# Optimization experiments

Hardware: AMD Instinct MI355X
Metric: run time of the kernel (lower is better)

## Reference

```python
import jax, jax.numpy as jnp
import numpy as np

N, E, D = 50000, 600000, 128


def setup_inputs() -> dict:
    key = jax.random.key(0)
    ks = jax.random.split(key, 7)
    s = 1.0 / np.sqrt(D)
    return {
        "x": jax.random.normal(ks[0], (N, D), dtype=jnp.float32),
        "edge_index": jax.random.randint(ks[1], (2, E), 0, N, dtype=jnp.int64),
        "Wl1": jax.random.normal(ks[2], (D, D), dtype=jnp.float32) * s,
        "Wr1": jax.random.normal(ks[3], (D, D), dtype=jnp.float32) * s,
        "b1": jnp.zeros((D,), dtype=jnp.float32),
        "Wl2": jax.random.normal(ks[4], (D, D), dtype=jnp.float32) * s,
        "Wr2": jax.random.normal(ks[5], (D, D), dtype=jnp.float32) * s,
        "b2": jnp.zeros((D,), dtype=jnp.float32),
    }


def _sage_conv(h, edge_index, Wl, Wr, b):
    # PyG SAGEConv (mean aggr): out = lin_l(mean_{j in N(i)} h_j) + lin_r(h_i)
    src, dst = edge_index[0], edge_index[1]
    n = h.shape[0]
    msg = h[src]                                            # [E, D] gather
    agg = jax.ops.segment_sum(msg, dst, num_segments=n)     # [N, D] scatter-add
    cnt = jax.ops.segment_sum(jnp.ones((src.shape[0],), h.dtype), dst,
                              num_segments=n)               # in-degree
    agg = agg / jnp.maximum(cnt, 1.0)[:, None]              # mean (0 for isolated)
    return agg @ Wl + h @ Wr + b


def reference(x, edge_index, Wl1, Wr1, b1, Wl2, Wr2, b2):
    h = jax.nn.relu(_sage_conv(x, edge_index, Wl1, Wr1, b1))
    # F.dropout(p=0.5) is identity in eval mode (deterministic baseline)
    return _sage_conv(h, edge_index, Wl2, Wr2, b2)
```

## Files before the change

### kernel.cpp

```cpp
#include <hip/hip_runtime.h>

typedef unsigned int u32;
typedef unsigned short u16;
typedef __attribute__((ext_vector_type(8))) short bf16x8;
typedef __attribute__((ext_vector_type(4))) float f32x4;

__device__ __forceinline__ u32 f2bf(float f) {
  u32 x = __float_as_uint(f);
  return (x + 0x7fffu + ((x >> 16) & 1u)) >> 16;
}
__device__ __forceinline__ float bf2f(u16 u) {
  return __uint_as_float(((u32)u) << 16);
}
__device__ __forceinline__ void addbf8(float* a, uint4 v) {
  a[0] += bf2f((u16)v.x); a[1] += bf2f((u16)(v.x >> 16));
  a[2] += bf2f((u16)v.y); a[3] += bf2f((u16)(v.y >> 16));
  a[4] += bf2f((u16)v.z); a[5] += bf2f((u16)(v.z >> 16));
  a[6] += bf2f((u16)v.w); a[7] += bf2f((u16)(v.w >> 16));
}

__global__ void setup_kernel(const float* __restrict__ Wl1, const float* __restrict__ Wr1,
                             const float* __restrict__ Wl2, const float* __restrict__ Wr2,
                             u16* __restrict__ G1, u16* __restrict__ G2,
                             int* __restrict__ cnt, int n) {
  int b = blockIdx.x;
  if (b < 256) {
    const float* Wl = (b < 128) ? Wl1 : Wl2;
    const float* Wr = (b < 128) ? Wr1 : Wr2;
    u16* G = (b < 128) ? G1 : G2;
    int id = (b & 127) * 256 + threadIdx.x;
    int c = id >> 7;
    int k = id & 127;
    const float* W = (c < 128) ? Wl : Wr;
    float v = W[k * 128 + (c & 127)];
    G[c * 128 + (k ^ ((c & 7) << 3))] = (u16)f2bf(v);
  } else {
    int i = (b - 256) * 256 + threadIdx.x;
    if (i < n) cnt[i] = 0;
  }
}

__global__ void hist_kernel(const int* __restrict__ dst, int* __restrict__ cnt,
                            int* __restrict__ pos, int E) {
  int e = blockIdx.x * blockDim.x + threadIdx.x;
  if (e < E) pos[e] = atomicAdd(&cnt[dst[e]], 1);
}

#define SCAN_CHUNK 2048

__global__ __launch_bounds__(256) void scan_sums(const int* __restrict__ cnt,
                                                 int* __restrict__ bsum, int n) {
  __shared__ int red[256];
  int t = threadIdx.x;
  int base = blockIdx.x * SCAN_CHUNK + t * 8;
  int s = 0;
#pragma unroll
  for (int i = 0; i < 8; ++i) {
    int idx = base + i;
    if (idx < n) s += cnt[idx];
  }
  red[t] = s;
  __syncthreads();
  for (int off = 128; off > 0; off >>= 1) {
    if (t < off) red[t] += red[t + off];
    __syncthreads();
  }
  if (t == 0) bsum[blockIdx.x] = red[0];
}

__global__ __launch_bounds__(256) void scan_apply(
    const int* __restrict__ cnt, const int* __restrict__ bsum, int nb,
    int* __restrict__ row_ptr, float* __restrict__ inv_cnt, int n) {
  __shared__ int sc[256];
  __shared__ int base_s;
  int t = threadIdx.x;
  if (t == 0) {
    int run = 0;
    int bid = blockIdx.x;
    int base = 0;
    for (int i = 0; i < nb; ++i) {
      if (i == bid) base = run;
      run += bsum[i];
    }
    base_s = base;
    if (bid == 0) row_ptr[n] = run;
  }
  int chunk_base = blockIdx.x * SCAN_CHUNK + t * 8;
  int v[8];
  int s = 0;
#pragma unroll
  for (int i = 0; i < 8; ++i) {
    int idx = chunk_base + i;
    v[i] = (idx < n) ? cnt[idx] : 0;
    s += v[i];
  }
  sc[t] = s;
  __syncthreads();
  for (int off = 1; off < 256; off <<= 1) {
    int add = (t >= off) ? sc[t - off] : 0;
    __syncthreads();
    sc[t] += add;
    __syncthreads();
  }
  int run = base_s + ((t > 0) ? sc[t - 1] : 0);
#pragma unroll
  for (int i = 0; i < 8; ++i) {
    int idx = chunk_base + i;
    if (idx < n) {
      row_ptr[idx] = run;
      inv_cnt[idx] = 1.0f / (float)max(v[i], 1);
      run += v[i];
    }
  }
}

template <int IN_BF16>
__device__ __forceinline__ void gemm_tiles(const void* in_, const u16* __restrict__ G,
                                           const float* __restrict__ bias,
                                           u16* __restrict__ yl, u16* __restrict__ yr,
                                           int n, uint4* lds4, int gb) {
  char* As = (char*)lds4;
  char* Bt = (char*)lds4 + 16384;
  const int t = threadIdx.x;
  const int lane = t & 63;
  const int wave = t >> 6;
  const int wr = wave >> 1;
  const int wc = wave & 1;
  const int lhi = lane >> 4;
  const int llo = lane & 15;

  {
    const uint4* gbp = (const uint4*)G;
    uint4* lb = lds4 + 1024;
#pragma unroll
    for (int i = 0; i < 16; ++i) lb[i * 256 + t] = gbp[i * 256 + t];
  }

  const int ntiles = (n + 63) / 64;
#pragma unroll 1
  for (int tile = gb * 2; tile < ntiles && tile < gb * 2 + 2; ++tile) {
    const int row0 = tile * 64;
    __syncthreads();
#pragma unroll
    for (int i = 0; i < 4; ++i) {
      int g = t + i * 256;
      int r = g >> 4;
      int gc = g & 15;
      int row = row0 + r;
      uint4 pk = {0u, 0u, 0u, 0u};
      if (row < n) {
        if (IN_BF16) {
          pk = *(const uint4*)((const u16*)in_ + (size_t)row * 128 + gc * 8);
        } else {
          const float4* pp = (const float4*)((const float*)in_ + (size_t)row * 128 + gc * 8);
          float4 v0 = pp[0], v1 = pp[1];
          pk.x = f2bf(v0.x) | (f2bf(v0.y) << 16);
          pk.y = f2bf(v0.z) | (f2bf(v0.w) << 16);
          pk.z = f2bf(v1.x) | (f2bf(v1.y) << 16);
          pk.w = f2bf(v1.z) | (f2bf(v1.w) << 16);
        }
      }
      *(uint4*)(As + r * 256 + ((gc * 16) ^ ((r & 7) << 4))) = pk;
    }
    __syncthreads();

    f32x4 acc[2][8];
#pragma unroll
    for (int fr = 0; fr < 2; ++fr)
#pragma unroll
      for (int fc = 0; fc < 8; ++fc) acc[fr][fc] = {0.f, 0.f, 0.f, 0.f};

#pragma unroll
    for (int ks = 0; ks < 4; ++ks) {
      const int kbyte = ks * 64 + lhi * 16;
      bf16x8 a[2], bb[8];
#pragma unroll
      for (int fr = 0; fr < 2; ++fr) {
        int r = wr * 32 + fr * 16 + llo;
        a[fr] = *(const bf16x8*)(As + r * 256 + (kbyte ^ ((r & 7) << 4)));
      }
#pragma unroll
      for (int fc = 0; fc < 8; ++fc) {
        int c = wc * 128 + fc * 16 + llo;
        bb[fc] = *(const bf16x8*)(Bt + c * 256 + (kbyte ^ ((c & 7) << 4)));
      }
#pragma unroll
      for (int fr = 0; fr < 2; ++fr)
#pragma unroll
        for (int fc = 0; fc < 8; ++fc)
          acc[fr][fc] = __builtin_amdgcn_mfma_f32_16x16x32_bf16(a[fr], bb[fc], acc[fr][fc], 0, 0, 0);
    }

#pragma unroll 1
    for (int ph = 0; ph < 2; ++ph) {
      __syncthreads();
      if (wc == ph) {
#pragma unroll
        for (int fc = 0; fc < 8; ++fc) {
          int cc = fc * 16 + llo;
          float bv = (ph == 1) ? bias[cc] : 0.0f;
#pragma unroll
          for (int fr = 0; fr < 2; ++fr) {
#pragma unroll
            for (int i = 0; i < 4; ++i) {
              int row = wr * 32 + fr * 16 + lhi * 4 + i;
              *(u16*)(As + row * 256 + ((cc * 2) ^ (lhi << 5))) =
                  (u16)f2bf(acc[fr][fc][i] + bv);
            }
          }
        }
      }
      __syncthreads();
      u16* outp = (ph == 0) ? yl : yr;
#pragma unroll
      for (int j = 0; j < 4; ++j) {
        int idx = t + j * 256;
        int row = idx >> 4;
        int cb = (idx & 15) * 16;
        int grow = row0 + row;
        if (grow < n) {
          uint4 v = *(const uint4*)(As + row * 256 + (cb ^ (((row >> 2) & 3) << 5)));
          *(uint4*)((char*)(outp + (size_t)grow * 128) + cb) = v;
        }
      }
    }
  }
}

__global__ __launch_bounds__(256, 2) void gemm1_fill_kernel(
    const float* __restrict__ x, const u16* __restrict__ G1, const float* __restrict__ b1,
    u16* __restrict__ yl, u16* __restrict__ yr, int n,
    const int* __restrict__ src, const int* __restrict__ dst,
    const int* __restrict__ pos, const int* __restrict__ row_ptr,
    int* __restrict__ colv, int E, int GB) {
  __shared__ uint4 lds4[5120];
  if ((int)blockIdx.x < GB) {
    gemm_tiles<0>(x, G1, b1, yl, yr, n, lds4, blockIdx.x);
  } else {
    int base = ((int)blockIdx.x - GB) * 2048 + threadIdx.x;
    int dd[8], pp[8], ss[8], rp[8];
#pragma unroll
    for (int j = 0; j < 8; ++j) {
      int e = base + j * 256;
      if (e < E) { dd[j] = dst[e]; pp[j] = pos[e]; ss[j] = src[e]; }
    }
#pragma unroll
    for (int j = 0; j < 8; ++j) {
      int e = base + j * 256;
      if (e < E) rp[j] = row_ptr[dd[j]];
    }
#pragma unroll
    for (int j = 0; j < 8; ++j) {
      int e = base + j * 256;
      if (e < E) colv[rp[j] + pp[j]] = ss[j];
    }
  }
}

template <int IN_BF16>
__global__ __launch_bounds__(256, 2) void gemm_kernel(
    const void* __restrict__ in_, const u16* __restrict__ G, const float* __restrict__ bias,
    u16* __restrict__ yl, u16* __restrict__ yr, int n) {
  __shared__ uint4 lds4[5120];
  gemm_tiles<IN_BF16>(in_, G, bias, yl, yr, n, lds4, blockIdx.x);
}

template <int RELU, int OUT_BF16>
__global__ __launch_bounds__(256) void agg_kernel(
    const u16* __restrict__ yl, const u16* __restrict__ yr,
    const int* __restrict__ row_ptr, const int* __restrict__ colv,
    const float* __restrict__ invc, void* __restrict__ out_, int n) {
  int node = blockIdx.x * 16 + (threadIdx.x >> 4);
  if (node >= n) return;
  int sl = threadIdx.x & 15;
  int beg = row_ptr[node], end = row_ptr[node + 1];
  uint4 rv = *(const uint4*)(yr + (size_t)node * 128 + sl * 8);
  float s = invc[node];
  float a[8] = {0.f, 0.f, 0.f, 0.f, 0.f, 0.f, 0.f, 0.f};
  for (int e0 = beg; e0 < end; e0 += 8) {
    int m = end - e0;
    if (m > 8) m = 8;
    uint4 v0, v1, v2, v3, v4, v5, v6, v7;
    if (0 < m) v0 = *(const uint4*)(yl + (size_t)colv[e0 + 0] * 128 + sl * 8);
    if (1 < m) v1 = *(const uint4*)(yl + (size_t)colv[e0 + 1] * 128 + sl * 8);
    if (2 < m) v2 = *(const uint4*)(yl + (size_t)colv[e0 + 2] * 128 + sl * 8);
    if (3 < m) v3 = *(const uint4*)(yl + (size_t)colv[e0 + 3] * 128 + sl * 8);
    if (4 < m) v4 = *(const uint4*)(yl + (size_t)colv[e0 + 4] * 128 + sl * 8);
    if (5 < m) v5 = *(const uint4*)(yl + (size_t)colv[e0 + 5] * 128 + sl * 8);
    if (6 < m) v6 = *(const uint4*)(yl + (size_t)colv[e0 + 6] * 128 + sl * 8);
    if (7 < m) v7 = *(const uint4*)(yl + (size_t)colv[e0 + 7] * 128 + sl * 8);
    if (0 < m) addbf8(a, v0);
    if (1 < m) addbf8(a, v1);
    if (2 < m) addbf8(a, v2);
    if (3 < m) addbf8(a, v3);
    if (4 < m) addbf8(a, v4);
    if (5 < m) addbf8(a, v5);
    if (6 < m) addbf8(a, v6);
    if (7 < m) addbf8(a, v7);
  }
  float r[8];
  r[0] = bf2f((u16)rv.x); r[1] = bf2f((u16)(rv.x >> 16));
  r[2] = bf2f((u16)rv.y); r[3] = bf2f((u16)(rv.y >> 16));
  r[4] = bf2f((u16)rv.z); r[5] = bf2f((u16)(rv.z >> 16));
  r[6] = bf2f((u16)rv.w); r[7] = bf2f((u16)(rv.w >> 16));
  float o[8];
#pragma unroll
  for (int j = 0; j < 8; ++j) {
    o[j] = a[j] * s + r[j];
    if (RELU) o[j] = fmaxf(o[j], 0.f);
  }
  if (OUT_BF16) {
    uint4 pk;
    pk.x = f2bf(o[0]) | (f2bf(o[1]) << 16);
    pk.y = f2bf(o[2]) | (f2bf(o[3]) << 16);
    pk.z = f2bf(o[4]) | (f2bf(o[5]) << 16);
    pk.w = f2bf(o[6]) | (f2bf(o[7]) << 16);
    *(uint4*)((u16*)out_ + (size_t)node * 128 + sl * 8) = pk;
  } else {
    float4 q0 = {o[0], o[1], o[2], o[3]};
    float4 q1 = {o[4], o[5], o[6], o[7]};
    float* op = (float*)out_ + (size_t)node * 128 + sl * 8;
    *(float4*)op = q0;
    *(float4*)(op + 4) = q1;
  }
}

extern "C" void kernel_launch(void* const* d_in, const int* in_sizes, int n_in,
                              void* d_out, int out_size, void* d_ws, size_t ws_size,
                              hipStream_t stream) {
  const float* x = (const float*)d_in[0];
  const int* ei = (const int*)d_in[1];
  const float* Wl1 = (const float*)d_in[2];
  const float* Wr1 = (const float*)d_in[3];
  const float* b1 = (const float*)d_in[4];
  const float* Wl2 = (const float*)d_in[5];
  const float* Wr2 = (const float*)d_in[6];
  const float* b2 = (const float*)d_in[7];

  const int N = in_sizes[0] / 128;
  const int E = in_sizes[1] / 2;
  const int* srcv = ei;
  const int* dstv = ei + E;

  char* ws = (char*)d_ws;
  u16* yl = (u16*)ws;       ws += (size_t)N * 128 * 2;
  u16* yr = (u16*)ws;       ws += (size_t)N * 128 * 2;
  u16* hbf = (u16*)ws;      ws += (size_t)N * 128 * 2;
  u16* G1 = (u16*)ws;       ws += 256 * 128 * 2;
  u16* G2 = (u16*)ws;       ws += 256 * 128 * 2;
  int* colv = (int*)ws;     ws += (size_t)E * 4;
  int* pos = (int*)ws;      ws += (size_t)E * 4;
  int* row_ptr = (int*)ws;  ws += ((size_t)N + 64) * 4;
  int* cnt = (int*)ws;      ws += (size_t)N * 4;
  float* invc = (float*)ws; ws += (size_t)N * 4;
  int* bsum = (int*)ws;     ws += 256 * 4;

  const int nsb = (N + SCAN_CHUNK - 1) / SCAN_CHUNK;
  const int ntiles = (N + 63) / 64;
  const int GB = (ntiles + 1) / 2;
  const int FB = (E + 2047) / 2048;

  setup_kernel<<<256 + (N + 255) / 256, 256, 0, stream>>>(Wl1, Wr1, Wl2, Wr2, G1, G2, cnt, N);
  hist_kernel<<<(E + 255) / 256, 256, 0, stream>>>(dstv, cnt, pos, E);
  scan_sums<<<nsb, 256, 0, stream>>>(cnt, bsum, N);
  scan_apply<<<nsb, 256, 0, stream>>>(cnt, bsum, nsb, row_ptr, invc, N);
  gemm1_fill_kernel<<<GB + FB, 256, 0, stream>>>(x, G1, b1, yl, yr, N,
                                                 srcv, dstv, pos, row_ptr, colv, E, GB);
  agg_kernel<1, 1><<<(N + 15) / 16, 256, 0, stream>>>(yl, yr, row_ptr, colv, invc, hbf, N);
  gemm_kernel<1><<<GB, 256, 0, stream>>>(hbf, G2, b2, yl, yr, N);
  agg_kernel<0, 0><<<(N + 15) / 16, 256, 0, stream>>>(yl, yr, row_ptr, colv, invc, d_out, N);
}
```

Before: 140.9 us.

## Split aggregation feature dimension into four column quarters across grid

The aggregation kernel now assigns 4 lanes per node covering a 32-column quarter, with the grid split into four passes over all nodes, one per quarter. Each pass gathers only a 64-byte slice of each neighbor row, so the gathered working set per pass is a quarter of the feature table and more likely to stay in L2/MALL. In exchange the row_ptr, colv and invc reads are repeated four times, and each gather is a 64-byte segment rather than a full 256-byte row.

```diff
diff --git a/kernel.cpp b/kernel.cpp
--- a/kernel.cpp
+++ b/kernel.cpp
@@ -269,26 +269,30 @@
 __global__ __launch_bounds__(256) void agg_kernel(
     const u16* __restrict__ yl, const u16* __restrict__ yr,
     const int* __restrict__ row_ptr, const int* __restrict__ colv,
-    const float* __restrict__ invc, void* __restrict__ out_, int n) {
-  int node = blockIdx.x * 16 + (threadIdx.x >> 4);
+    const float* __restrict__ invc, void* __restrict__ out_, int n, int nb) {
+  int q = blockIdx.x / nb;
+  int nblk = blockIdx.x - q * nb;
+  int node = nblk * 64 + (threadIdx.x >> 2);
   if (node >= n) return;
-  int sl = threadIdx.x & 15;
+  int l4 = threadIdx.x & 3;
+  int co = q * 32 + l4 * 8;
+  const u16* ylq = yl + co;
   int beg = row_ptr[node], end = row_ptr[node + 1];
-  uint4 rv = *(const uint4*)(yr + (size_t)node * 128 + sl * 8);
+  uint4 rv = *(const uint4*)(yr + (size_t)node * 128 + co);
   float s = invc[node];
   float a[8] = {0.f, 0.f, 0.f, 0.f, 0.f, 0.f, 0.f, 0.f};
   for (int e0 = beg; e0 < end; e0 += 8) {
     int m = end - e0;
     if (m > 8) m = 8;
     uint4 v0, v1, v2, v3, v4, v5, v6, v7;
-    if (0 < m) v0 = *(const uint4*)(yl + (size_t)colv[e0 + 0] * 128 + sl * 8);
-    if (1 < m) v1 = *(const uint4*)(yl + (size_t)colv[e0 + 1] * 128 + sl * 8);
-    if (2 < m) v2 = *(const uint4*)(yl + (size_t)colv[e0 + 2] * 128 + sl * 8);
-    if (3 < m) v3 = *(const uint4*)(yl + (size_t)colv[e0 + 3] * 128 + sl * 8);
-    if (4 < m) v4 = *(const uint4*)(yl + (size_t)colv[e0 + 4] * 128 + sl * 8);
-    if (5 < m) v5 = *(const uint4*)(yl + (size_t)colv[e0 + 5] * 128 + sl * 8);
-    if (6 < m) v6 = *(const uint4*)(yl + (size_t)colv[e0 + 6] * 128 + sl * 8);
-    if (7 < m) v7 = *(const uint4*)(yl + (size_t)colv[e0 + 7] * 128 + sl * 8);
+    if (0 < m) v0 = *(const uint4*)(ylq + (size_t)colv[e0 + 0] * 128);
+    if (1 < m) v1 = *(const uint4*)(ylq + (size_t)colv[e0 + 1] * 128);
+    if (2 < m) v2 = *(const uint4*)(ylq + (size_t)colv[e0 + 2] * 128);
+    if (3 < m) v3 = *(const uint4*)(ylq + (size_t)colv[e0 + 3] * 128);
+    if (4 < m) v4 = *(const uint4*)(ylq + (size_t)colv[e0 + 4] * 128);
+    if (5 < m) v5 = *(const uint4*)(ylq + (size_t)colv[e0 + 5] * 128);
+    if (6 < m) v6 = *(const uint4*)(ylq + (size_t)colv[e0 + 6] * 128);
+    if (7 < m) v7 = *(const uint4*)(ylq + (size_t)colv[e0 + 7] * 128);
     if (0 < m) addbf8(a, v0);
     if (1 < m) addbf8(a, v1);
     if (2 < m) addbf8(a, v2);
@@ -315,11 +319,11 @@
     pk.y = f2bf(o[2]) | (f2bf(o[3]) << 16);
     pk.z = f2bf(o[4]) | (f2bf(o[5]) << 16);
     pk.w = f2bf(o[6]) | (f2bf(o[7]) << 16);
-    *(uint4*)((u16*)out_ + (size_t)node * 128 + sl * 8) = pk;
+    *(uint4*)((u16*)out_ + (size_t)node * 128 + co) = pk;
   } else {
     float4 q0 = {o[0], o[1], o[2], o[3]};
     float4 q1 = {o[4], o[5], o[6], o[7]};
-    float* op = (float*)out_ + (size_t)node * 128 + sl * 8;
+    float* op = (float*)out_ + (size_t)node * 128 + co;
     *(float4*)op = q0;
     *(float4*)(op + 4) = q1;
   }
@@ -359,6 +363,7 @@
   const int ntiles = (N + 63) / 64;
   const int GB = (ntiles + 1) / 2;
   const int FB = (E + 2047) / 2048;
+  const int nbq = (N + 63) / 64;
 
   setup_kernel<<<256 + (N + 255) / 256, 256, 0, stream>>>(Wl1, Wr1, Wl2, Wr2, G1, G2, cnt, N);
   hist_kernel<<<(E + 255) / 256, 256, 0, stream>>>(dstv, cnt, pos, E);
@@ -366,7 +371,7 @@
   scan_apply<<<nsb, 256, 0, stream>>>(cnt, bsum, nsb, row_ptr, invc, N);
   gemm1_fill_kernel<<<GB + FB, 256, 0, stream>>>(x, G1, b1, yl, yr, N,
                                                  srcv, dstv, pos, row_ptr, colv, E, GB);
-  agg_kernel<1, 1><<<(N + 15) / 16, 256, 0, stream>>>(yl, yr, row_ptr, colv, invc, hbf, N);
+  agg_kernel<1, 1><<<4 * nbq, 256, 0, stream>>>(yl, yr, row_ptr, colv, invc, hbf, N, nbq);
   gemm_kernel<1><<<GB, 256, 0, stream>>>(hbf, G2, b2, yl, yr, N);
-  agg_kernel<0, 0><<<(N + 15) / 16, 256, 0, stream>>>(yl, yr, row_ptr, colv, invc, d_out, N);
-}
+  agg_kernel<0, 0><<<4 * nbq, 256, 0, stream>>>(yl, yr, row_ptr, colv, invc, d_out, N, nbq);
+}
```

Result: slower. 167.8 us (+19.1%).
